# Kernel tuning notes

Hardware: AMD Instinct MI355X
Metric: run time of the kernel (lower is better)

Reference implementation:

```python
import jax, jax.numpy as jnp
import numpy as np

B = 4096          # graphs
NPG = 50          # nodes per graph
N = B * NPG       # total nodes
E = 819200        # edges
C = 128           # hidden_channels
T = 2048          # num_tools


def setup_inputs() -> dict:
    key = jax.random.key(0)
    ks = jax.random.split(key, 12)
    s = 0.1
    return {
        "x": jax.random.randint(ks[0], (N, 1), 0, T, dtype=jnp.int32),
        "edge_index": jax.random.randint(ks[1], (2, E), 0, N, dtype=jnp.int32),
        "batch": (jnp.arange(N, dtype=jnp.int32) // NPG).astype(jnp.int32),
        "num_graphs": B,
        "embedding": jax.random.normal(ks[2], (T, C), jnp.float32) * s,
        "w_ih": jax.random.normal(ks[3], (3 * C, C), jnp.float32) * s,
        "w_hh": jax.random.normal(ks[4], (3 * C, C), jnp.float32) * s,
        "w1": jax.random.normal(ks[5], (C, C), jnp.float32) * s,
        "w2": jax.random.normal(ks[6], (C, C), jnp.float32) * s,
        "b2": jax.random.normal(ks[7], (C,), jnp.float32) * s,
        "wq": jax.random.normal(ks[8], (C, C), jnp.float32) * s,
        "bq": jax.random.normal(ks[9], (C,), jnp.float32) * s,
        "wt": jax.random.normal(ks[10], (C, 2 * C), jnp.float32) * s,
    }


def reference(x, edge_index, batch, num_graphs, embedding, w_ih, w_hh,
              w1, w2, b2, wq, bq, wt):
    n = x.shape[0]
    # embedding lookup (dropout2d is identity at eval)
    emb = embedding[x[:, 0]]                                   # [N, C]

    # --- GatedGraphConv: scatter-add of source features to targets ---
    src, dst = edge_index[0], edge_index[1]
    m = jax.ops.segment_sum(emb[src], dst, num_segments=n)     # [N, C]

    # --- GRUCell(m, emb), no bias ---
    gi = m @ w_ih.T                                            # [N, 3C]
    gh = emb @ w_hh.T                                          # [N, 3C]
    i_r, i_z, i_n = jnp.split(gi, 3, axis=1)
    h_r, h_z, h_n = jnp.split(gh, 3, axis=1)
    r = jax.nn.sigmoid(i_r + h_r)
    z = jax.nn.sigmoid(i_z + h_z)
    ncand = jnp.tanh(i_n + r * h_n)
    h = (1.0 - z) * ncand + z * emb                            # [N, C]

    # --- ragged segment attention readout ---
    counts = jax.ops.segment_sum(jnp.ones_like(batch), batch,
                                 num_segments=num_graphs)      # [B]
    last_idx = jnp.cumsum(counts) - 1                          # [B]
    w_l = h[last_idx]                                          # [B, C] last node per graph
    w_g_r = w_l[batch]                                         # [N, C] broadcast to nodes
    q1 = w_g_r @ w1.T
    q2 = h @ w2.T + b2
    alpha = jax.nn.sigmoid(q1 + q2) @ wq.T + bq                # [N, C]
    w_g = jax.ops.segment_sum(alpha * h, batch,
                              num_segments=num_graphs)         # [B, C]

    w = jnp.concatenate([w_l, w_g], axis=1) @ wt.T             # [B, C]
    logits = w @ embedding.T                                   # [B, T]
    return logits
```

## Files before the change

kernel.cpp:

```cpp
#include <hip/hip_runtime.h>
#include <hip/hip_bf16.h>

#define NN 204800
#define EE 819200
#define BB 4096
#define NPG 50
#define CC 128
#define TT 2048
#define BINCAP 32

typedef __attribute__((ext_vector_type(8))) short short8;
typedef __attribute__((ext_vector_type(4))) float f32x4;

__device__ __forceinline__ short f2bf(float f) {
    union { float f; unsigned u; } v; v.f = f;
    unsigned r = (v.u + 0x7FFFu + ((v.u >> 16) & 1u)) >> 16;
    return (short)r;
}
__device__ __forceinline__ float bf2f(short s) {
    union { float f; unsigned u; } v;
    v.u = ((unsigned)(unsigned short)s) << 16;
    return v.f;
}
__device__ __forceinline__ float sigf(float x) { return 1.0f / (1.0f + __expf(-x)); }
__device__ __forceinline__ float tanh_fast(float x) {
    x = fminf(fmaxf(x, -15.0f), 15.0f);
    float e = __expf(2.0f * x);
    return 1.0f - 2.0f / (e + 1.0f);
}

__global__ void prep_small(const float* __restrict__ emb, const float* __restrict__ w1,
                           const float* __restrict__ w2, const float* __restrict__ wq,
                           const float* __restrict__ wt,
                           __hip_bfloat16* __restrict__ embbf, __hip_bfloat16* __restrict__ w1bf,
                           __hip_bfloat16* __restrict__ w2bf, __hip_bfloat16* __restrict__ wqbf,
                           __hip_bfloat16* __restrict__ wtbf) {
    int i = blockIdx.x * 256 + threadIdx.x;
    if (i < TT * CC) embbf[i] = __float2bfloat16(emb[i]);
    if (i < CC * CC) {
        w1bf[i] = __float2bfloat16(w1[i]);
        w2bf[i] = __float2bfloat16(w2[i]);
        wqbf[i] = __float2bfloat16(wq[i]);
    }
    if (i < CC * 2 * CC) wtbf[i] = __float2bfloat16(wt[i]);
}

__global__ __launch_bounds__(256) void build_tables(const float* __restrict__ emb,
                                                    const float* __restrict__ w_ih,
                                                    const float* __restrict__ w_hh,
                                                    __hip_bfloat16* __restrict__ G_ih,
                                                    __hip_bfloat16* __restrict__ G_hh) {
    __shared__ float wch[CC][CC + 1];
    __shared__ float et[16][CC];
    int t = threadIdx.x;
    int tokbase = blockIdx.x * 16;
    int chunk = blockIdx.y;
    const float* w = (chunk < 3) ? w_ih : w_hh;
    __hip_bfloat16* G = (chunk < 3) ? G_ih : G_hh;
    int jbase = (chunk % 3) * CC;
    for (int idx = t; idx < CC * CC; idx += 256) {
        int j = idx >> 7, k = idx & 127;
        wch[j][k] = w[(jbase + j) * CC + k];
    }
    for (int idx = t; idx < 16 * CC; idx += 256) {
        int tok = idx >> 7, k = idx & 127;
        et[tok][k] = emb[(tokbase + tok) * CC + k];
    }
    __syncthreads();
    int j = t & 127, grp = t >> 7;
    float acc[8];
#pragma unroll
    for (int u = 0; u < 8; u++) acc[u] = 0.f;
    for (int k = 0; k < CC; k++) {
        float wv = wch[j][k];
#pragma unroll
        for (int u = 0; u < 8; u++) acc[u] += et[grp * 8 + u][k] * wv;
    }
#pragma unroll
    for (int u = 0; u < 8; u++)
        G[(tokbase + grp * 8 + u) * 384 + jbase + j] = __float2bfloat16(acc[u]);
}

__global__ void fill_bins(const int* __restrict__ ei, const int* __restrict__ x,
                          int* __restrict__ deg, int* __restrict__ bins) {
    int e = blockIdx.x * 256 + threadIdx.x;
    int d = ei[EE + e], s = ei[e];
    int pos = atomicAdd(&deg[d], 1);
    bins[(size_t)d * BINCAP + pos] = x[s];
}

__global__ __launch_bounds__(256) void gru_kernel(
    const int* __restrict__ x, const int* __restrict__ deg,
    const int* __restrict__ bins,
    const __hip_bfloat16* __restrict__ G_ih, const __hip_bfloat16* __restrict__ G_hh,
    const float* __restrict__ emb,
    __hip_bfloat16* __restrict__ hbf) {
    int nid = blockIdx.x * 16 + (threadIdx.x >> 4);
    int j = threadIdx.x & 15;
    int tok = x[nid];
    int dg = deg[nid];
    const int* bin = bins + (size_t)nid * BINCAP;
    float ir[8], iz[8], inn[8];
#pragma unroll
    for (int p = 0; p < 8; p++) { ir[p] = 0.f; iz[p] = 0.f; inn[p] = 0.f; }
    for (int c = 0; c < dg; c += 4) {
        int4 tq = *(const int4*)&bin[c];
        int tks[4] = {tq.x, tq.y, tq.z, tq.w};
#pragma unroll
        for (int u = 0; u < 4; u++) {
            if (c + u < dg) {
                int st = tks[u];
                const short8* gp = (const short8*)(G_ih + (size_t)st * 384);
                short8 a = gp[j];
                short8 b = gp[16 + j];
                short8 c2 = gp[32 + j];
#pragma unroll
                for (int p = 0; p < 8; p++) {
                    ir[p]  += bf2f(a[p]);
                    iz[p]  += bf2f(b[p]);
                    inn[p] += bf2f(c2[p]);
                }
            }
        }
    }
    const short8* hp = (const short8*)(G_hh + (size_t)tok * 384);
    short8 hr = hp[j], hz = hp[16 + j], hn = hp[32 + j];
    const float4* ep = (const float4*)(emb + (size_t)tok * CC + j * 8);
    float4 ev0 = ep[0], ev1 = ep[1];
    float evs[8] = {ev0.x, ev0.y, ev0.z, ev0.w, ev1.x, ev1.y, ev1.z, ev1.w};
    short8 hv;
#pragma unroll
    for (int p = 0; p < 8; p++) {
        float r  = sigf(ir[p] + bf2f(hr[p]));
        float z  = sigf(iz[p] + bf2f(hz[p]));
        float nc = tanh_fast(inn[p] + r * bf2f(hn[p]));
        float h  = (1.f - z) * nc + z * evs[p];
        hv[p] = f2bf(h);
    }
    ((short8*)hbf)[nid * 16 + j] = hv;
}

__global__ __launch_bounds__(256, 4) void graph4(
    const __hip_bfloat16* __restrict__ hbf,
    const __hip_bfloat16* __restrict__ w1bf, const __hip_bfloat16* __restrict__ w2bf,
    const __hip_bfloat16* __restrict__ wqbf,
    const float* __restrict__ b2, const float* __restrict__ bq,
    __hip_bfloat16* __restrict__ w_lbf, __hip_bfloat16* __restrict__ w_gbf) {
    __shared__ short hsb[64][CC + 8];
    __shared__ short ssb[64][CC + 8];
    int g = blockIdx.x, t = threadIdx.x;

    const short8* hsrc = (const short8*)(hbf + (size_t)g * NPG * CC);
    for (int idx = t; idx < NPG * 16; idx += 256)
        *(short8*)&hsb[idx >> 4][(idx & 15) * 8] = hsrc[idx];
    {
        short8 z8 = (short8){0,0,0,0,0,0,0,0};
        short8* tail = (short8*)&hsb[NPG][0];
        for (int idx = t; idx < 14 * 17; idx += 256) tail[idx] = z8;
    }
    __syncthreads();

    int wave = t >> 6, lane = t & 63;
    int mrow = lane & 15, quad = lane >> 4;
    int colb = wave * 32;

    if (t < 16)
        *(short8*)(w_lbf + (size_t)g * CC + t * 8) = *(const short8*)&hsb[NPG - 1][t * 8];

    f32x4 acc[4][2];
#pragma unroll
    for (int n = 0; n < 2; n++) {
        int col = colb + n * 16 + mrow;
        float bv = b2[col];
        f32x4 a0 = (f32x4){bv, bv, bv, bv};
#pragma unroll
        for (int kt = 0; kt < 4; kt++) {
            short8 aq = *(const short8*)&hsb[NPG - 1][kt * 32 + quad * 8];
            short8 bw1 = *(const short8*)(w1bf + (size_t)col * CC + kt * 32 + quad * 8);
            a0 = __builtin_amdgcn_mfma_f32_16x16x32_bf16(aq, bw1, a0, 0, 0, 0);
        }
#pragma unroll
        for (int rt = 0; rt < 4; rt++) acc[rt][n] = a0;
    }
    {
        short8 bw2[2][4];
#pragma unroll
        for (int n = 0; n < 2; n++)
#pragma unroll
            for (int kt = 0; kt < 4; kt++)
                bw2[n][kt] = *(const short8*)(w2bf + (size_t)(colb + n * 16 + mrow) * CC + kt * 32 + quad * 8);
#pragma unroll
        for (int kt = 0; kt < 4; kt++)
#pragma unroll
            for (int rt = 0; rt < 4; rt++) {
                short8 af = *(const short8*)&hsb[rt * 16 + mrow][kt * 32 + quad * 8];
#pragma unroll
                for (int n = 0; n < 2; n++)
                    acc[rt][n] = __builtin_amdgcn_mfma_f32_16x16x32_bf16(af, bw2[n][kt], acc[rt][n], 0, 0, 0);
            }
    }
#pragma unroll
    for (int rt = 0; rt < 4; rt++)
#pragma unroll
        for (int n = 0; n < 2; n++)
#pragma unroll
            for (int r = 0; r < 4; r++)
                ssb[rt * 16 + quad * 4 + r][colb + n * 16 + mrow] = f2bf(sigf(acc[rt][n][r]));
    __syncthreads();

    f32x4 acd[4][2];
    short8 bwq[2][4];
#pragma unroll
    for (int n = 0; n < 2; n++) {
        float bv = bq[colb + n * 16 + mrow];
#pragma unroll
        for (int rt = 0; rt < 4; rt++) acd[rt][n] = (f32x4){bv, bv, bv, bv};
#pragma unroll
        for (int kt = 0; kt < 4; kt++)
            bwq[n][kt] = *(const short8*)(wqbf + (size_t)(colb + n * 16 + mrow) * CC + kt * 32 + quad * 8);
    }
#pragma unroll
    for (int kt = 0; kt < 4; kt++)
#pragma unroll
        for (int rt = 0; rt < 4; rt++) {
            short8 af = *(const short8*)&ssb[rt * 16 + mrow][kt * 32 + quad * 8];
#pragma unroll
            for (int n = 0; n < 2; n++)
                acd[rt][n] = __builtin_amdgcn_mfma_f32_16x16x32_bf16(af, bwq[n][kt], acd[rt][n], 0, 0, 0);
        }
#pragma unroll
    for (int n = 0; n < 2; n++) {
        int col = colb + n * 16 + mrow;
        float ps = 0.f;
#pragma unroll
        for (int rt = 0; rt < 4; rt++)
#pragma unroll
            for (int r = 0; r < 4; r++)
                ps += acd[rt][n][r] * bf2f(hsb[rt * 16 + quad * 4 + r][col]);
        ps += __shfl_xor(ps, 16, 64);
        ps += __shfl_xor(ps, 32, 64);
        if (quad == 0) w_gbf[(size_t)g * CC + col] = __float2bfloat16(ps);
    }
}

__global__ __launch_bounds__(256) void out_gemm(
    const __hip_bfloat16* __restrict__ w_lbf, const __hip_bfloat16* __restrict__ w_gbf,
    const __hip_bfloat16* __restrict__ wtbf, const __hip_bfloat16* __restrict__ embbf,
    float* __restrict__ out) {
    __shared__ float wvs[64][CC + 4];
    int t = threadIdx.x;
    int gbase = blockIdx.x * 64;
    int tbase = blockIdx.y * 256;
    int wave = t >> 6, lane = t & 63;
    int mrow = lane & 15, quad = lane >> 4;

    f32x4 acc[8];
#pragma unroll
    for (int nt = 0; nt < 8; nt++) acc[nt] = (f32x4){0.f, 0.f, 0.f, 0.f};
    int grow = gbase + wave * 16 + mrow;
#pragma unroll
    for (int kt = 0; kt < 8; kt++) {
        const __hip_bfloat16* asrc = (kt < 4)
            ? (w_lbf + grow * CC + kt * 32 + quad * 8)
            : (w_gbf + grow * CC + (kt - 4) * 32 + quad * 8);
        short8 af = *(const short8*)asrc;
#pragma unroll
        for (int nt = 0; nt < 8; nt++) {
            const short8* bp = (const short8*)(wtbf + (nt * 16 + mrow) * 256 + kt * 32 + quad * 8);
            acc[nt] = __builtin_amdgcn_mfma_f32_16x16x32_bf16(af, *bp, acc[nt], 0, 0, 0);
        }
    }
#pragma unroll
    for (int nt = 0; nt < 8; nt++)
#pragma unroll
        for (int r = 0; r < 4; r++)
            wvs[wave * 16 + quad * 4 + r][nt * 16 + mrow] = acc[nt][r];
    __syncthreads();

    f32x4 acc3[16];
#pragma unroll
    for (int nt = 0; nt < 16; nt++) acc3[nt] = (f32x4){0.f, 0.f, 0.f, 0.f};
#pragma unroll
    for (int kt = 0; kt < 4; kt++) {
        const float* ap = &wvs[wave * 16 + mrow][kt * 32 + quad * 8];
        short8 af;
#pragma unroll
        for (int j2 = 0; j2 < 8; j2++) af[j2] = f2bf(ap[j2]);
#pragma unroll
        for (int nt = 0; nt < 16; nt++) {
            const short8* bp = (const short8*)(embbf + (tbase + nt * 16 + mrow) * CC + kt * 32 + quad * 8);
            acc3[nt] = __builtin_amdgcn_mfma_f32_16x16x32_bf16(af, *bp, acc3[nt], 0, 0, 0);
        }
    }
#pragma unroll
    for (int nt = 0; nt < 16; nt++)
#pragma unroll
        for (int r = 0; r < 4; r++) {
            int grow2 = gbase + wave * 16 + quad * 4 + r;
            int tok = tbase + nt * 16 + mrow;
            out[grow2 * TT + tok] = acc3[nt][r];
        }
}

extern "C" void kernel_launch(void* const* d_in, const int* in_sizes, int n_in,
                              void* d_out, int out_size, void* d_ws, size_t ws_size,
                              hipStream_t stream) {
    const int* x     = (const int*)d_in[0];
    const int* ei    = (const int*)d_in[1];
    const float* emb = (const float*)d_in[4];
    const float* w_ih = (const float*)d_in[5];
    const float* w_hh = (const float*)d_in[6];
    const float* w1  = (const float*)d_in[7];
    const float* w2  = (const float*)d_in[8];
    const float* b2  = (const float*)d_in[9];
    const float* wq  = (const float*)d_in[10];
    const float* bq  = (const float*)d_in[11];
    const float* wt  = (const float*)d_in[12];
    float* out = (float*)d_out;

    char* ws = (char*)d_ws;
    size_t off = 0;
    auto alloc = [&](size_t b) { void* p = ws + off; off += (b + 255) & ~(size_t)255; return p; };
    __hip_bfloat16* G_ih  = (__hip_bfloat16*)alloc((size_t)TT * 384 * 2);
    __hip_bfloat16* G_hh  = (__hip_bfloat16*)alloc((size_t)TT * 384 * 2);
    __hip_bfloat16* embbf = (__hip_bfloat16*)alloc((size_t)TT * CC * 2);
    __hip_bfloat16* w1bf  = (__hip_bfloat16*)alloc((size_t)CC * CC * 2);
    __hip_bfloat16* w2bf  = (__hip_bfloat16*)alloc((size_t)CC * CC * 2);
    __hip_bfloat16* wqbf  = (__hip_bfloat16*)alloc((size_t)CC * CC * 2);
    __hip_bfloat16* wtbf  = (__hip_bfloat16*)alloc((size_t)CC * 256 * 2);
    int* deg              = (int*)alloc((size_t)NN * 4);
    int* bins             = (int*)alloc((size_t)NN * BINCAP * 4);
    __hip_bfloat16* w_lbf = (__hip_bfloat16*)alloc((size_t)BB * CC * 2);
    __hip_bfloat16* w_gbf = (__hip_bfloat16*)alloc((size_t)BB * CC * 2);
    __hip_bfloat16* hbf   = (__hip_bfloat16*)alloc((size_t)NN * CC * 2);

    hipMemsetAsync(deg, 0, (size_t)NN * 4, stream);
    prep_small<<<1024, 256, 0, stream>>>(emb, w1, w2, wq, wt, embbf, w1bf, w2bf, wqbf, wtbf);
    build_tables<<<dim3(TT / 16, 6), 256, 0, stream>>>(emb, w_ih, w_hh, G_ih, G_hh);
    fill_bins<<<EE / 256, 256, 0, stream>>>(ei, x, deg, bins);
    gru_kernel<<<NN / 16, 256, 0, stream>>>(x, deg, bins, G_ih, G_hh, emb, hbf);
    graph4<<<BB, 256, 0, stream>>>(hbf, w1bf, w2bf, wqbf, b2, bq, w_lbf, w_gbf);
    out_gemm<<<dim3(BB / 64, TT / 256), 256, 0, stream>>>(w_lbf, w_gbf, wtbf, embbf, out);
}
```

Before: 324.5 us.

## Gather raw embeddings then apply W_ih via MFMA instead of precomputed G_ih table

Instead of precomputing per-token input-gate projections (G_ih, 384 wide) and gathering three 128-wide rows per edge, the GRU kernel now gathers 128-wide bf16 embedding rows per edge, sums them into an LDS tile of 32 nodes, and multiplies by W_ih with bf16 MFMA. This cuts the per-edge gather traffic to a third and drops half of the table-building work. In exchange it adds a per-block GEMM, rounds the message sum to bf16 before the projection, and issues scalar, non-vectorized epilogue stores and G_hh loads.

Result: slower. 386.5 us (+19.1%).

```diff
diff --git a/kernel.cpp b/kernel.cpp
--- a/kernel.cpp
+++ b/kernel.cpp
@@ -31,10 +31,10 @@
 
 __global__ void prep_small(const float* __restrict__ emb, const float* __restrict__ w1,
                            const float* __restrict__ w2, const float* __restrict__ wq,
-                           const float* __restrict__ wt,
+                           const float* __restrict__ wt, const float* __restrict__ w_ih,
                            __hip_bfloat16* __restrict__ embbf, __hip_bfloat16* __restrict__ w1bf,
                            __hip_bfloat16* __restrict__ w2bf, __hip_bfloat16* __restrict__ wqbf,
-                           __hip_bfloat16* __restrict__ wtbf) {
+                           __hip_bfloat16* __restrict__ wtbf, __hip_bfloat16* __restrict__ w_ihbf) {
     int i = blockIdx.x * 256 + threadIdx.x;
     if (i < TT * CC) embbf[i] = __float2bfloat16(emb[i]);
     if (i < CC * CC) {
@@ -43,24 +43,21 @@
         wqbf[i] = __float2bfloat16(wq[i]);
     }
     if (i < CC * 2 * CC) wtbf[i] = __float2bfloat16(wt[i]);
+    if (i < 3 * CC * CC) w_ihbf[i] = __float2bfloat16(w_ih[i]);
 }
 
 __global__ __launch_bounds__(256) void build_tables(const float* __restrict__ emb,
-                                                    const float* __restrict__ w_ih,
                                                     const float* __restrict__ w_hh,
-                                                    __hip_bfloat16* __restrict__ G_ih,
                                                     __hip_bfloat16* __restrict__ G_hh) {
     __shared__ float wch[CC][CC + 1];
     __shared__ float et[16][CC];
     int t = threadIdx.x;
     int tokbase = blockIdx.x * 16;
     int chunk = blockIdx.y;
-    const float* w = (chunk < 3) ? w_ih : w_hh;
-    __hip_bfloat16* G = (chunk < 3) ? G_ih : G_hh;
-    int jbase = (chunk % 3) * CC;
+    int jbase = chunk * CC;
     for (int idx = t; idx < CC * CC; idx += 256) {
         int j = idx >> 7, k = idx & 127;
-        wch[j][k] = w[(jbase + j) * CC + k];
+        wch[j][k] = w_hh[(jbase + j) * CC + k];
     }
     for (int idx = t; idx < 16 * CC; idx += 256) {
         int tok = idx >> 7, k = idx & 127;
@@ -78,7 +75,7 @@
     }
 #pragma unroll
     for (int u = 0; u < 8; u++)
-        G[(tokbase + grp * 8 + u) * 384 + jbase + j] = __float2bfloat16(acc[u]);
+        G_hh[(tokbase + grp * 8 + u) * 384 + jbase + j] = __float2bfloat16(acc[u]);
 }
 
 __global__ void fill_bins(const int* __restrict__ ei, const int* __restrict__ x,
@@ -89,55 +86,101 @@
     bins[(size_t)d * BINCAP + pos] = x[s];
 }
 
-__global__ __launch_bounds__(256) void gru_kernel(
-    const int* __restrict__ x, const int* __restrict__ deg,
-    const int* __restrict__ bins,
-    const __hip_bfloat16* __restrict__ G_ih, const __hip_bfloat16* __restrict__ G_hh,
-    const float* __restrict__ emb,
+__global__ __launch_bounds__(256, 3) void gru2(
+    const int* __restrict__ x, const int* __restrict__ deg, const int* __restrict__ bins,
+    const __hip_bfloat16* __restrict__ embbf, const __hip_bfloat16* __restrict__ G_hh,
+    const __hip_bfloat16* __restrict__ w_ihbf,
     __hip_bfloat16* __restrict__ hbf) {
-    int nid = blockIdx.x * 16 + (threadIdx.x >> 4);
-    int j = threadIdx.x & 15;
-    int tok = x[nid];
-    int dg = deg[nid];
-    const int* bin = bins + (size_t)nid * BINCAP;
-    float ir[8], iz[8], inn[8];
-#pragma unroll
-    for (int p = 0; p < 8; p++) { ir[p] = 0.f; iz[p] = 0.f; inn[p] = 0.f; }
-    for (int c = 0; c < dg; c += 4) {
-        int4 tq = *(const int4*)&bin[c];
-        int tks[4] = {tq.x, tq.y, tq.z, tq.w};
-#pragma unroll
-        for (int u = 0; u < 4; u++) {
-            if (c + u < dg) {
-                int st = tks[u];
-                const short8* gp = (const short8*)(G_ih + (size_t)st * 384);
-                short8 a = gp[j];
-                short8 b = gp[16 + j];
-                short8 c2 = gp[32 + j];
-#pragma unroll
-                for (int p = 0; p < 8; p++) {
-                    ir[p]  += bf2f(a[p]);
-                    iz[p]  += bf2f(b[p]);
-                    inn[p] += bf2f(c2[p]);
+    __shared__ short mt[32][CC + 8];
+    __shared__ int stok[32];
+    int t = threadIdx.x;
+    int nb = blockIdx.x * 32;
+    if (t < 32) stok[t] = x[nb + t];
+
+#pragma unroll
+    for (int chunk = 0; chunk < 2; chunk++) {
+        int node = chunk * 16 + (t >> 4);
+        int j = t & 15;
+        int nid = nb + node;
+        int dg = deg[nid];
+        const int* bin = bins + (size_t)nid * BINCAP;
+        float a8[8];
+#pragma unroll
+        for (int p = 0; p < 8; p++) a8[p] = 0.f;
+        for (int c = 0; c < dg; c += 4) {
+            int4 tq = *(const int4*)&bin[c];
+            int tks[4] = {tq.x, tq.y, tq.z, tq.w};
+#pragma unroll
+            for (int u = 0; u < 4; u++) {
+                if (c + u < dg) {
+                    short8 ev = ((const short8*)(embbf + (size_t)tks[u] * CC))[j];
+#pragma unroll
+                    for (int p = 0; p < 8; p++) a8[p] += bf2f(ev[p]);
                 }
             }
         }
-    }
-    const short8* hp = (const short8*)(G_hh + (size_t)tok * 384);
-    short8 hr = hp[j], hz = hp[16 + j], hn = hp[32 + j];
-    const float4* ep = (const float4*)(emb + (size_t)tok * CC + j * 8);
-    float4 ev0 = ep[0], ev1 = ep[1];
-    float evs[8] = {ev0.x, ev0.y, ev0.z, ev0.w, ev1.x, ev1.y, ev1.z, ev1.w};
-    short8 hv;
-#pragma unroll
-    for (int p = 0; p < 8; p++) {
-        float r  = sigf(ir[p] + bf2f(hr[p]));
-        float z  = sigf(iz[p] + bf2f(hz[p]));
-        float nc = tanh_fast(inn[p] + r * bf2f(hn[p]));
-        float h  = (1.f - z) * nc + z * evs[p];
-        hv[p] = f2bf(h);
-    }
-    ((short8*)hbf)[nid * 16 + j] = hv;
+        short8 mv;
+#pragma unroll
+        for (int p = 0; p < 8; p++) mv[p] = f2bf(a8[p]);
+        *(short8*)&mt[node][j * 8] = mv;
+    }
+    __syncthreads();
+
+    int wave = t >> 6, lane = t & 63;
+    int mrow = lane & 15, quad = lane >> 4;
+    int colb = wave * 32;
+
+    f32x4 acc[3][2][2];
+#pragma unroll
+    for (int g = 0; g < 3; g++)
+#pragma unroll
+        for (int rt = 0; rt < 2; rt++)
+#pragma unroll
+            for (int n = 0; n < 2; n++) acc[g][rt][n] = (f32x4){0.f, 0.f, 0.f, 0.f};
+#pragma unroll
+    for (int kt = 0; kt < 4; kt++) {
+        short8 bw[3][2];
+#pragma unroll
+        for (int g = 0; g < 3; g++)
+#pragma unroll
+            for (int n = 0; n < 2; n++)
+                bw[g][n] = *(const short8*)(w_ihbf +
+                    (size_t)(g * CC + colb + n * 16 + mrow) * CC + kt * 32 + quad * 8);
+#pragma unroll
+        for (int rt = 0; rt < 2; rt++) {
+            short8 af = *(const short8*)&mt[rt * 16 + mrow][kt * 32 + quad * 8];
+#pragma unroll
+            for (int g = 0; g < 3; g++)
+#pragma unroll
+                for (int n = 0; n < 2; n++)
+                    acc[g][rt][n] = __builtin_amdgcn_mfma_f32_16x16x32_bf16(af, bw[g][n], acc[g][rt][n], 0, 0, 0);
+        }
+    }
+
+    const unsigned short* ghp = (const unsigned short*)G_hh;
+    const unsigned short* ebp = (const unsigned short*)embbf;
+#pragma unroll
+    for (int rt = 0; rt < 2; rt++)
+#pragma unroll
+        for (int r = 0; r < 4; r++) {
+            int row = rt * 16 + quad * 4 + r;
+            int tokr = stok[row];
+            size_t gb = (size_t)tokr * 384;
+            size_t eb = (size_t)tokr * CC;
+#pragma unroll
+            for (int n = 0; n < 2; n++) {
+                int c = colb + n * 16 + mrow;
+                float ir  = acc[0][rt][n][r] + bf2f((short)ghp[gb + c]);
+                float iz  = acc[1][rt][n][r] + bf2f((short)ghp[gb + 128 + c]);
+                float hn  = bf2f((short)ghp[gb + 256 + c]);
+                float rr  = sigf(ir);
+                float zz  = sigf(iz);
+                float nc  = tanh_fast(acc[2][rt][n][r] + rr * hn);
+                float ev  = bf2f((short)ebp[eb + c]);
+                float h   = (1.f - zz) * nc + zz * ev;
+                hbf[(size_t)(nb + row) * CC + c] = __float2bfloat16(h);
+            }
+        }
 }
 
 __global__ __launch_bounds__(256, 4) void graph4(
@@ -321,13 +364,13 @@
     char* ws = (char*)d_ws;
     size_t off = 0;
     auto alloc = [&](size_t b) { void* p = ws + off; off += (b + 255) & ~(size_t)255; return p; };
-    __hip_bfloat16* G_ih  = (__hip_bfloat16*)alloc((size_t)TT * 384 * 2);
     __hip_bfloat16* G_hh  = (__hip_bfloat16*)alloc((size_t)TT * 384 * 2);
     __hip_bfloat16* embbf = (__hip_bfloat16*)alloc((size_t)TT * CC * 2);
     __hip_bfloat16* w1bf  = (__hip_bfloat16*)alloc((size_t)CC * CC * 2);
     __hip_bfloat16* w2bf  = (__hip_bfloat16*)alloc((size_t)CC * CC * 2);
     __hip_bfloat16* wqbf  = (__hip_bfloat16*)alloc((size_t)CC * CC * 2);
     __hip_bfloat16* wtbf  = (__hip_bfloat16*)alloc((size_t)CC * 256 * 2);
+    __hip_bfloat16* w_ihbf= (__hip_bfloat16*)alloc((size_t)3 * CC * CC * 2);
     int* deg              = (int*)alloc((size_t)NN * 4);
     int* bins             = (int*)alloc((size_t)NN * BINCAP * 4);
     __hip_bfloat16* w_lbf = (__hip_bfloat16*)alloc((size_t)BB * CC * 2);
@@ -335,10 +378,11 @@
     __hip_bfloat16* hbf   = (__hip_bfloat16*)alloc((size_t)NN * CC * 2);
 
     hipMemsetAsync(deg, 0, (size_t)NN * 4, stream);
-    prep_small<<<1024, 256, 0, stream>>>(emb, w1, w2, wq, wt, embbf, w1bf, w2bf, wqbf, wtbf);
-    build_tables<<<dim3(TT / 16, 6), 256, 0, stream>>>(emb, w_ih, w_hh, G_ih, G_hh);
+    prep_small<<<1024, 256, 0, stream>>>(emb, w1, w2, wq, wt, w_ih,
+                                         embbf, w1bf, w2bf, wqbf, wtbf, w_ihbf);
+    build_tables<<<dim3(TT / 16, 3), 256, 0, stream>>>(emb, w_hh, G_hh);
     fill_bins<<<EE / 256, 256, 0, stream>>>(ei, x, deg, bins);
-    gru_kernel<<<NN / 16, 256, 0, stream>>>(x, deg, bins, G_ih, G_hh, emb, hbf);
+    gru2<<<NN / 32, 256, 0, stream>>>(x, deg, bins, embbf, G_hh, w_ihbf, hbf);
     graph4<<<BB, 256, 0, stream>>>(hbf, w1bf, w2bf, wqbf, b2, bq, w_lbf, w_gbf);
     out_gemm<<<dim3(BB / 64, TT / 256), 256, 0, stream>>>(w_lbf, w_gbf, wtbf, embbf, out);
 }
```

## Pack node rows densely across graphs and split readout into separate GEMM kernels

Applied to the files above, without the earlier changes.

The per-graph attention kernel, which padded each 50-node graph to a 64-row tile, is replaced by a node-tiled kernel that processes 64 contiguous nodes per block. That removes the padding waste. Each block adds a precomputed per-graph q1 bias and accumulates the per-graph sums with float atomics across at most three graphs. The q1 projection and the wt projection now run in their own small kernels, and the logits GEMM uses smaller N-tiles with the A operand staged in shared memory. The cost is extra launches, a memset, fp32 intermediates, atomic traffic and non-deterministic summation order.

Measured after the change: 308.8 us. -4.8%, faster.

```diff
diff --git a/kernel.cpp b/kernel.cpp
--- a/kernel.cpp
+++ b/kernel.cpp
@@ -140,23 +140,58 @@
     ((short8*)hbf)[nid * 16 + j] = hv;
 }
 
-__global__ __launch_bounds__(256, 4) void graph4(
-    const __hip_bfloat16* __restrict__ hbf,
-    const __hip_bfloat16* __restrict__ w1bf, const __hip_bfloat16* __restrict__ w2bf,
-    const __hip_bfloat16* __restrict__ wqbf,
-    const float* __restrict__ b2, const float* __restrict__ bq,
-    __hip_bfloat16* __restrict__ w_lbf, __hip_bfloat16* __restrict__ w_gbf) {
+__global__ __launch_bounds__(256) void q1_kernel(
+    const __hip_bfloat16* __restrict__ hbf, const __hip_bfloat16* __restrict__ w1bf,
+    const float* __restrict__ b2,
+    float* __restrict__ q1_all, __hip_bfloat16* __restrict__ w_lbf) {
+    int t = threadIdx.x;
+    int gbase = blockIdx.x * 64;
+    int wave = t >> 6, lane = t & 63;
+    int mrow = lane & 15, quad = lane >> 4;
+    int g = gbase + wave * 16 + mrow;
+
+    short8 afr[4];
+#pragma unroll
+    for (int kt = 0; kt < 4; kt++) {
+        afr[kt] = *(const short8*)(hbf + ((size_t)g * NPG + NPG - 1) * CC + kt * 32 + quad * 8);
+        *(short8*)(w_lbf + (size_t)g * CC + kt * 32 + quad * 8) = afr[kt];
+    }
+    f32x4 acc[8];
+#pragma unroll
+    for (int nt = 0; nt < 8; nt++) {
+        float bv = b2[nt * 16 + mrow];
+        acc[nt] = (f32x4){bv, bv, bv, bv};
+    }
+#pragma unroll
+    for (int kt = 0; kt < 4; kt++) {
+#pragma unroll
+        for (int nt = 0; nt < 8; nt++) {
+            const short8* bp = (const short8*)(w1bf + (nt * 16 + mrow) * CC + kt * 32 + quad * 8);
+            acc[nt] = __builtin_amdgcn_mfma_f32_16x16x32_bf16(afr[kt], *bp, acc[nt], 0, 0, 0);
+        }
+    }
+#pragma unroll
+    for (int nt = 0; nt < 8; nt++)
+#pragma unroll
+        for (int r = 0; r < 4; r++)
+            q1_all[(size_t)(gbase + wave * 16 + quad * 4 + r) * CC + nt * 16 + mrow] = acc[nt][r];
+}
+
+__global__ __launch_bounds__(256, 4) void node_attn(
+    const __hip_bfloat16* __restrict__ hbf, const float* __restrict__ q1_all,
+    const __hip_bfloat16* __restrict__ w2bf, const __hip_bfloat16* __restrict__ wqbf,
+    const float* __restrict__ bq,
+    float* __restrict__ w_gf) {
     __shared__ short hsb[64][CC + 8];
     __shared__ short ssb[64][CC + 8];
-    int g = blockIdx.x, t = threadIdx.x;
-
-    const short8* hsrc = (const short8*)(hbf + (size_t)g * NPG * CC);
-    for (int idx = t; idx < NPG * 16; idx += 256)
+    int rb = blockIdx.x * 64;
+    int t = threadIdx.x;
+
+    const short8* hsrc = (const short8*)(hbf + (size_t)rb * CC);
+#pragma unroll
+    for (int it = 0; it < 4; it++) {
+        int idx = it * 256 + t;
         *(short8*)&hsb[idx >> 4][(idx & 15) * 8] = hsrc[idx];
-    {
-        short8 z8 = (short8){0,0,0,0,0,0,0,0};
-        short8* tail = (short8*)&hsb[NPG][0];
-        for (int idx = t; idx < 14 * 17; idx += 256) tail[idx] = z8;
     }
     __syncthreads();
 
@@ -164,24 +199,11 @@
     int mrow = lane & 15, quad = lane >> 4;
     int colb = wave * 32;
 
-    if (t < 16)
-        *(short8*)(w_lbf + (size_t)g * CC + t * 8) = *(const short8*)&hsb[NPG - 1][t * 8];
-
     f32x4 acc[4][2];
 #pragma unroll
-    for (int n = 0; n < 2; n++) {
-        int col = colb + n * 16 + mrow;
-        float bv = b2[col];
-        f32x4 a0 = (f32x4){bv, bv, bv, bv};
-#pragma unroll
-        for (int kt = 0; kt < 4; kt++) {
-            short8 aq = *(const short8*)&hsb[NPG - 1][kt * 32 + quad * 8];
-            short8 bw1 = *(const short8*)(w1bf + (size_t)col * CC + kt * 32 + quad * 8);
-            a0 = __builtin_amdgcn_mfma_f32_16x16x32_bf16(aq, bw1, a0, 0, 0, 0);
-        }
-#pragma unroll
-        for (int rt = 0; rt < 4; rt++) acc[rt][n] = a0;
-    }
+    for (int rt = 0; rt < 4; rt++)
+#pragma unroll
+        for (int n = 0; n < 2; n++) acc[rt][n] = (f32x4){0.f, 0.f, 0.f, 0.f};
     {
         short8 bw2[2][4];
 #pragma unroll
@@ -204,8 +226,12 @@
 #pragma unroll
         for (int n = 0; n < 2; n++)
 #pragma unroll
-            for (int r = 0; r < 4; r++)
-                ssb[rt * 16 + quad * 4 + r][colb + n * 16 + mrow] = f2bf(sigf(acc[rt][n][r]));
+            for (int r = 0; r < 4; r++) {
+                int rowl = rt * 16 + quad * 4 + r;
+                int col = colb + n * 16 + mrow;
+                int g = (rb + rowl) / 50;
+                ssb[rowl][col] = f2bf(sigf(acc[rt][n][r] + q1_all[(size_t)g * CC + col]));
+            }
     __syncthreads();
 
     f32x4 acd[4][2];
@@ -228,42 +254,58 @@
             for (int n = 0; n < 2; n++)
                 acd[rt][n] = __builtin_amdgcn_mfma_f32_16x16x32_bf16(af, bwq[n][kt], acd[rt][n], 0, 0, 0);
         }
+    int g0 = rb / 50;
+    int gmax = (rb + 63) / 50;
 #pragma unroll
     for (int n = 0; n < 2; n++) {
         int col = colb + n * 16 + mrow;
-        float ps = 0.f;
+        float ps0 = 0.f, ps1 = 0.f, ps2 = 0.f;
 #pragma unroll
         for (int rt = 0; rt < 4; rt++)
 #pragma unroll
-            for (int r = 0; r < 4; r++)
-                ps += acd[rt][n][r] * bf2f(hsb[rt * 16 + quad * 4 + r][col]);
-        ps += __shfl_xor(ps, 16, 64);
-        ps += __shfl_xor(ps, 32, 64);
-        if (quad == 0) w_gbf[(size_t)g * CC + col] = __float2bfloat16(ps);
-    }
-}
-
-__global__ __launch_bounds__(256) void out_gemm(
-    const __hip_bfloat16* __restrict__ w_lbf, const __hip_bfloat16* __restrict__ w_gbf,
-    const __hip_bfloat16* __restrict__ wtbf, const __hip_bfloat16* __restrict__ embbf,
-    float* __restrict__ out) {
-    __shared__ float wvs[64][CC + 4];
+            for (int r = 0; r < 4; r++) {
+                int rowl = rt * 16 + quad * 4 + r;
+                int gg = (rb + rowl) / 50;
+                float v = acd[rt][n][r] * bf2f(hsb[rowl][col]);
+                ps0 += (gg == g0)     ? v : 0.f;
+                ps1 += (gg == g0 + 1) ? v : 0.f;
+                ps2 += (gg == g0 + 2) ? v : 0.f;
+            }
+        ps0 += __shfl_xor(ps0, 16, 64); ps0 += __shfl_xor(ps0, 32, 64);
+        ps1 += __shfl_xor(ps1, 16, 64); ps1 += __shfl_xor(ps1, 32, 64);
+        ps2 += __shfl_xor(ps2, 16, 64); ps2 += __shfl_xor(ps2, 32, 64);
+        if (quad == 0) {
+            atomicAdd(&w_gf[(size_t)g0 * CC + col], ps0);
+            if (g0 + 1 <= gmax) atomicAdd(&w_gf[(size_t)(g0 + 1) * CC + col], ps1);
+            if (g0 + 2 <= gmax) atomicAdd(&w_gf[(size_t)(g0 + 2) * CC + col], ps2);
+        }
+    }
+}
+
+__global__ __launch_bounds__(256) void wvec_kernel(
+    const __hip_bfloat16* __restrict__ w_lbf, const float* __restrict__ w_gf,
+    const __hip_bfloat16* __restrict__ wtbf,
+    __hip_bfloat16* __restrict__ wvecbf) {
     int t = threadIdx.x;
     int gbase = blockIdx.x * 64;
-    int tbase = blockIdx.y * 256;
     int wave = t >> 6, lane = t & 63;
     int mrow = lane & 15, quad = lane >> 4;
+    int grow = gbase + wave * 16 + mrow;
 
     f32x4 acc[8];
 #pragma unroll
     for (int nt = 0; nt < 8; nt++) acc[nt] = (f32x4){0.f, 0.f, 0.f, 0.f};
-    int grow = gbase + wave * 16 + mrow;
 #pragma unroll
     for (int kt = 0; kt < 8; kt++) {
-        const __hip_bfloat16* asrc = (kt < 4)
-            ? (w_lbf + grow * CC + kt * 32 + quad * 8)
-            : (w_gbf + grow * CC + (kt - 4) * 32 + quad * 8);
-        short8 af = *(const short8*)asrc;
+        short8 af;
+        if (kt < 4) {
+            af = *(const short8*)(w_lbf + (size_t)grow * CC + kt * 32 + quad * 8);
+        } else {
+            const float* ws = w_gf + (size_t)grow * CC + (kt - 4) * 32 + quad * 8;
+            float4 v0 = *(const float4*)ws, v1 = *(const float4*)(ws + 4);
+            af[0] = f2bf(v0.x); af[1] = f2bf(v0.y); af[2] = f2bf(v0.z); af[3] = f2bf(v0.w);
+            af[4] = f2bf(v1.x); af[5] = f2bf(v1.y); af[6] = f2bf(v1.z); af[7] = f2bf(v1.w);
+        }
 #pragma unroll
         for (int nt = 0; nt < 8; nt++) {
             const short8* bp = (const short8*)(wtbf + (nt * 16 + mrow) * 256 + kt * 32 + quad * 8);
@@ -274,31 +316,48 @@
     for (int nt = 0; nt < 8; nt++)
 #pragma unroll
         for (int r = 0; r < 4; r++)
-            wvs[wave * 16 + quad * 4 + r][nt * 16 + mrow] = acc[nt][r];
+            wvecbf[(size_t)(gbase + wave * 16 + quad * 4 + r) * CC + nt * 16 + mrow] =
+                __float2bfloat16(acc[nt][r]);
+}
+
+__global__ __launch_bounds__(256) void logits_kernel(
+    const __hip_bfloat16* __restrict__ wvecbf, const __hip_bfloat16* __restrict__ embbf,
+    float* __restrict__ out) {
+    __shared__ short avs[64][CC + 8];
+    int t = threadIdx.x;
+    int gbase = blockIdx.x * 64;
+    int tbase = blockIdx.y * 128;
+
+    const short8* asrc = (const short8*)(wvecbf + (size_t)gbase * CC);
+#pragma unroll
+    for (int it = 0; it < 4; it++) {
+        int idx = it * 256 + t;
+        *(short8*)&avs[idx >> 4][(idx & 15) * 8] = asrc[idx];
+    }
     __syncthreads();
 
-    f32x4 acc3[16];
-#pragma unroll
-    for (int nt = 0; nt < 16; nt++) acc3[nt] = (f32x4){0.f, 0.f, 0.f, 0.f};
+    int wave = t >> 6, lane = t & 63;
+    int mrow = lane & 15, quad = lane >> 4;
+
+    f32x4 acc3[8];
+#pragma unroll
+    for (int nt = 0; nt < 8; nt++) acc3[nt] = (f32x4){0.f, 0.f, 0.f, 0.f};
 #pragma unroll
     for (int kt = 0; kt < 4; kt++) {
-        const float* ap = &wvs[wave * 16 + mrow][kt * 32 + quad * 8];
-        short8 af;
-#pragma unroll
-        for (int j2 = 0; j2 < 8; j2++) af[j2] = f2bf(ap[j2]);
-#pragma unroll
-        for (int nt = 0; nt < 16; nt++) {
-            const short8* bp = (const short8*)(embbf + (tbase + nt * 16 + mrow) * CC + kt * 32 + quad * 8);
+        short8 af = *(const short8*)&avs[wave * 16 + mrow][kt * 32 + quad * 8];
+#pragma unroll
+        for (int nt = 0; nt < 8; nt++) {
+            const short8* bp = (const short8*)(embbf + (size_t)(tbase + nt * 16 + mrow) * CC + kt * 32 + quad * 8);
             acc3[nt] = __builtin_amdgcn_mfma_f32_16x16x32_bf16(af, *bp, acc3[nt], 0, 0, 0);
         }
     }
 #pragma unroll
-    for (int nt = 0; nt < 16; nt++)
+    for (int nt = 0; nt < 8; nt++)
 #pragma unroll
         for (int r = 0; r < 4; r++) {
             int grow2 = gbase + wave * 16 + quad * 4 + r;
             int tok = tbase + nt * 16 + mrow;
-            out[grow2 * TT + tok] = acc3[nt][r];
+            out[(size_t)grow2 * TT + tok] = acc3[nt][r];
         }
 }
 
@@ -331,14 +390,19 @@
     int* deg              = (int*)alloc((size_t)NN * 4);
     int* bins             = (int*)alloc((size_t)NN * BINCAP * 4);
     __hip_bfloat16* w_lbf = (__hip_bfloat16*)alloc((size_t)BB * CC * 2);
-    __hip_bfloat16* w_gbf = (__hip_bfloat16*)alloc((size_t)BB * CC * 2);
+    float* w_gf           = (float*)alloc((size_t)BB * CC * 4);
+    float* q1_all         = (float*)alloc((size_t)BB * CC * 4);
+    __hip_bfloat16* wvecbf= (__hip_bfloat16*)alloc((size_t)BB * CC * 2);
     __hip_bfloat16* hbf   = (__hip_bfloat16*)alloc((size_t)NN * CC * 2);
 
     hipMemsetAsync(deg, 0, (size_t)NN * 4, stream);
+    hipMemsetAsync(w_gf, 0, (size_t)BB * CC * 4, stream);
     prep_small<<<1024, 256, 0, stream>>>(emb, w1, w2, wq, wt, embbf, w1bf, w2bf, wqbf, wtbf);
     build_tables<<<dim3(TT / 16, 6), 256, 0, stream>>>(emb, w_ih, w_hh, G_ih, G_hh);
     fill_bins<<<EE / 256, 256, 0, stream>>>(ei, x, deg, bins);
     gru_kernel<<<NN / 16, 256, 0, stream>>>(x, deg, bins, G_ih, G_hh, emb, hbf);
-    graph4<<<BB, 256, 0, stream>>>(hbf, w1bf, w2bf, wqbf, b2, bq, w_lbf, w_gbf);
-    out_gemm<<<dim3(BB / 64, TT / 256), 256, 0, stream>>>(w_lbf, w_gbf, wtbf, embbf, out);
-}
+    q1_kernel<<<BB / 64, 256, 0, stream>>>(hbf, w1bf, b2, q1_all, w_lbf);
+    node_attn<<<NN / 64, 256, 0, stream>>>(hbf, q1_all, w2bf, wqbf, bq, w_gf);
+    wvec_kernel<<<BB / 64, 256, 0, stream>>>(w_lbf, w_gf, wtbf, wvecbf);
+    logits_kernel<<<dim3(BB / 64, TT / 128), 256, 0, stream>>>(wvecbf, embbf, out);
+}
```
